# Optimization experiments

Measured on AMD Instinct MI355X. Metric: run time of the kernel, lower is better.

## Reference

```python
import jax, jax.numpy as jnp
import numpy as np

B, S, D, H, L, V = 4, 512, 1024, 16, 4, 32000
DH = D // H
LATENT_START, N_LATENT, LATENT_ID = 64, 6, 5


def _ln(x, g, b):
    m = x.mean(-1, keepdims=True)
    v = ((x - m) ** 2).mean(-1, keepdims=True)
    return (x - m) * jax.lax.rsqrt(v + 1e-5) * g + b


def _model(x_emb, pos_ids, pos_emb, Wqkv, Wo, W1, W2, ln1_g, ln1_b, ln2_g, ln2_b, lnf_g, lnf_b, lm_head):
    # x_emb: [B,T,D]; returns (last_hidden [B,T,D] after final LN, logits [B,T,V])
    b, T, _ = x_emb.shape
    x = x_emb + pos_emb[pos_ids]
    causal = jnp.tril(jnp.ones((T, T), bool))
    for l in range(L):
        h = _ln(x, ln1_g[l], ln1_b[l])
        q, k, v = jnp.split(h @ Wqkv[l], 3, axis=-1)
        q = q.reshape(b, T, H, DH).transpose(0, 2, 1, 3)
        k = k.reshape(b, T, H, DH).transpose(0, 2, 1, 3)
        v = v.reshape(b, T, H, DH).transpose(0, 2, 1, 3)
        scores = jnp.einsum('bhqd,bhkd->bhqk', q, k) / np.float32(np.sqrt(DH))
        scores = jnp.where(causal, scores, jnp.float32(-1e9))
        attn = jax.nn.softmax(scores, axis=-1)
        o = jnp.einsum('bhqk,bhkd->bhqd', attn, v).transpose(0, 2, 1, 3).reshape(b, T, D)
        x = x + o @ Wo[l]
        h2 = _ln(x, ln2_g[l], ln2_b[l])
        x = x + jax.nn.gelu(h2 @ W1[l]) @ W2[l]
    hid = _ln(x, lnf_g, lnf_b)  # GPT2 hidden_states[-1] is post ln_f
    return hid, hid @ lm_head


def setup_inputs() -> dict:
    key = jax.random.key(0)
    ks = jax.random.split(key, 10)
    input_ids = jax.random.randint(ks[0], (B, S), 0, V, dtype=jnp.int32)
    input_ids = input_ids.at[:, LATENT_START:LATENT_START + N_LATENT].set(LATENT_ID)
    attention_mask = jnp.ones((B, S), jnp.int32)
    labels = jax.random.randint(ks[1], (B, S), 0, V, dtype=jnp.int32)
    position_ids = jnp.broadcast_to(jnp.arange(S, dtype=jnp.int32), (B, S))
    s = 0.02
    return {
        'input_ids': input_ids, 'attention_mask': attention_mask,
        'labels': labels, 'position_ids': position_ids,
        'emb': jax.random.normal(ks[2], (V, D), jnp.float32) * s,
        'pos_emb': jax.random.normal(ks[3], (S, D), jnp.float32) * s,
        'Wqkv': jax.random.normal(ks[4], (L, D, 3 * D), jnp.float32) * s,
        'Wo': jax.random.normal(ks[5], (L, D, D), jnp.float32) * s,
        'W1': jax.random.normal(ks[6], (L, D, 4 * D), jnp.float32) * s,
        'W2': jax.random.normal(ks[7], (L, 4 * D, D), jnp.float32) * s,
        'ln1_g': jnp.ones((L, D), jnp.float32), 'ln1_b': jnp.zeros((L, D), jnp.float32),
        'ln2_g': jnp.ones((L, D), jnp.float32), 'ln2_b': jnp.zeros((L, D), jnp.float32),
        'lnf_g': jnp.ones((D,), jnp.float32), 'lnf_b': jnp.zeros((D,), jnp.float32),
        'lm_head': jax.random.normal(ks[8], (D, V), jnp.float32) * s,
    }


def reference(input_ids, attention_mask, labels, position_ids, emb, pos_emb, Wqkv, Wo, W1, W2, ln1_g, ln1_b, ln2_g, ln2_b, lnf_g, lnf_b, lm_head):
    params = (pos_emb, Wqkv, Wo, W1, W2, ln1_g, ln1_b, ln2_g, ln2_b, lnf_g, lnf_b, lm_head)
    inputs_embeds = emb[input_ids]  # [B,S,D]
    start, end = 0, LATENT_START
    logits_list = []
    for p in range(N_LATENT):  # iterative latent passes
        hid, lg = _model(inputs_embeds[:, :end], position_ids[:, :end], *params)
        logits_list.append(lg[:, start:end])
        pos = LATENT_START + p
        # vectorized scatter: splice previous-position hidden state into latent slot
        inputs_embeds = inputs_embeds.at[:, pos, :].set(hid[:, pos - 1, :])
        start, end = end, (S if p + 1 >= N_LATENT else end + 1)
    hid, lg = _model(inputs_embeds[:, :end], position_ids[:, :end], *params)
    logits_list.append(lg[:, start:end])
    logits = jnp.concatenate(logits_list, axis=1)  # [B,S,V]
    shift_logits = logits[:, :-1]
    shift_labels = labels[:, 1:]
    logp = jax.nn.log_softmax(shift_logits, axis=-1)
    loss = -jnp.take_along_axis(logp, shift_labels[..., None], axis=-1).mean()
    return loss, inputs_embeds, logits
```

## Files before the change

### kernel.cpp

```cpp
#include <hip/hip_runtime.h>

static constexpr int BB  = 4;
static constexpr int SS  = 512;
static constexpr int DD  = 1024;
static constexpr int HH  = 16;
static constexpr int LL  = 4;
static constexpr int VV  = 32000;
static constexpr int DHH = 64;
static constexpr int FFF = 4096;

typedef short bf16x8  __attribute__((ext_vector_type(8)));
typedef short bf16x4v __attribute__((ext_vector_type(4)));
typedef float f32x4   __attribute__((ext_vector_type(4)));

__device__ __forceinline__ float b2f(ushort u){
  union { float f; unsigned int u32; } x; x.u32 = ((unsigned int)u) << 16; return x.f;
}
__device__ __forceinline__ ushort f2b(float f){
  union { float f; unsigned int u32; } x; x.f = f;
  unsigned int u = x.u32;
  return (ushort)((u + 0x7FFFu + ((u >> 16) & 1u)) >> 16);
}

__device__ __forceinline__ void gl_lds16(const void* gp, void* lp){
  __builtin_amdgcn_global_load_lds((const __attribute__((address_space(1))) unsigned int*)gp,
                                   (__attribute__((address_space(3))) unsigned int*)lp, 16, 0, 0);
}

__device__ __forceinline__ bf16x4v lds_read4(const void* buf, int row, int col){
  int byte = row * 128 + (((((col >> 3) ^ (row & 7)) << 4) | ((col & 7) << 1)));
  return *(const bf16x4v*)((const char*)buf + byte);
}

__global__ __launch_bounds__(256) void convT_k(const float* __restrict__ in, ushort* __restrict__ out,
                                               int K, int N, long inStride, long outStride)
{
  in  += (long)blockIdx.z * inStride;
  out += (long)blockIdx.z * outStride;
  __shared__ float tile[64][65];
  int n0 = blockIdx.x * 64, k0 = blockIdx.y * 64;
  int tid = threadIdx.x;
  int cc = tid & 63, rr = tid >> 6;
#pragma unroll
  for (int i = 0; i < 16; i++){
    int r = rr + i * 4;
    tile[r][cc] = in[(long)(k0 + r) * N + n0 + cc];
  }
  __syncthreads();
#pragma unroll
  for (int i = 0; i < 16; i++){
    int r = rr + i * 4;
    out[(long)(n0 + r) * K + k0 + cc] = f2b(tile[cc][r]);
  }
}

__global__ __launch_bounds__(256) void embed_k(const int* __restrict__ ids, const float* __restrict__ emb,
                                               const float* __restrict__ pe, float* __restrict__ x,
                                               float* __restrict__ oemb)
{
  int t = blockIdx.x, b = blockIdx.y, tid = threadIdx.x;
  int id = ids[b * SS + t];
  float4 ev = *((const float4*)(emb + (long)id * DD) + tid);
  float4 pv = *((const float4*)(pe  + (long)t  * DD) + tid);
  *((float4*)(x + (long)(t * BB + b) * DD) + tid) =
      make_float4(ev.x + pv.x, ev.y + pv.y, ev.z + pv.z, ev.w + pv.w);
  float* op = oemb + ((long)b * SS + t) * DD + tid * 4;
  op[0] = ev.x; op[1] = ev.y; op[2] = ev.z; op[3] = ev.w;
}

__global__ __launch_bounds__(256) void ln_k(const float* __restrict__ xin, const float* __restrict__ g,
                                            const float* __restrict__ bt, ushort* __restrict__ out, long row0)
{
  long row = row0 + blockIdx.x;
  int tid = threadIdx.x;
  const float* rp = xin + row * DD;
  float4 v = *(const float4*)(rp + tid * 4);
  float s1 = v.x + v.y + v.z + v.w;
  float s2 = v.x * v.x + v.y * v.y + v.z * v.z + v.w * v.w;
#pragma unroll
  for (int o = 32; o; o >>= 1){ s1 += __shfl_down(s1, o); s2 += __shfl_down(s2, o); }
  __shared__ float red[2][4];
  int wv = tid >> 6, lane = tid & 63;
  if (lane == 0){ red[0][wv] = s1; red[1][wv] = s2; }
  __syncthreads();
  s1 = red[0][0] + red[0][1] + red[0][2] + red[0][3];
  s2 = red[1][0] + red[1][1] + red[1][2] + red[1][3];
  float mean = s1 * (1.0f / DD);
  float var  = s2 * (1.0f / DD) - mean * mean;
  float rstd = rsqrtf(var + 1e-5f);
  float4 gv = *(const float4*)(g + tid * 4);
  float4 bv = *(const float4*)(bt + tid * 4);
  ushort4 o4;
  o4.x = f2b((v.x - mean) * rstd * gv.x + bv.x);
  o4.y = f2b((v.y - mean) * rstd * gv.y + bv.y);
  o4.z = f2b((v.z - mean) * rstd * gv.z + bv.z);
  o4.w = f2b((v.w - mean) * rstd * gv.w + bv.w);
  *(ushort4*)(out + row * DD + tid * 4) = o4;
}

template<int EPI>
__device__ __forceinline__ void epi_store(float v, int grow, int ocol, void* Cv, int ldc,
                                          const float* Add, int t0, int l,
                                          ushort* kc, ushort* vc, ushort* qb)
{
  if constexpr (EPI == 1){
    float* Cf = (float*)Cv; long idx = (long)grow * ldc + ocol;
    Cf[idx] = v + Add[idx];
  } else if constexpr (EPI == 2){
    ushort* Cb = (ushort*)Cv; long idx = (long)grow * ldc + ocol;
    float tt = 0.7978845608028654f * (v + 0.044715f * v * v * v);
    Cb[idx] = f2b(0.5f * v * (1.0f + tanhf(tt)));
  } else if constexpr (EPI == 3){
    int t = t0 + (grow >> 2), b = grow & 3;
    ((float*)Cv)[((long)b * SS + t) * VV + ocol] = v;
  } else if constexpr (EPI == 4){
    if (ocol < DD){
      qb[((long)(t0 * BB + grow)) * DD + ocol] = f2b(v);
    } else {
      int t = t0 + (grow >> 2), b = grow & 3;
      int h = (ocol >> 6) & 15, d = ocol & 63;
      long dst = (((long)l * BB + b) * HH + h) * ((long)SS * DHH) + (long)t * DHH + d;
      if (ocol >= 2 * DD) vc[dst] = f2b(v); else kc[dst] = f2b(v);
    }
  }
}

template<int EPI>
__global__ __launch_bounds__(256) void gemm_k(const ushort* __restrict__ A, int lda,
                                              const ushort* __restrict__ BT,
                                              void* Cv, int ldc,
                                              const float* Add,
                                              int M, int N, int K, int gx,
                                              int l, int t0,
                                              ushort* kc, ushort* vc, ushort* qb,
                                              float* part, int KS)
{
  constexpr int BM  = 128;
  constexpr int MFR = 4;
  constexpr int NFR = 4;
  __shared__ ushort As[BM][64];
  __shared__ ushort Bs[128][64];
  int tid = threadIdx.x;
  int wv = tid >> 6, lane = tid & 63;
  int wm = wv >> 1, wn = wv & 1;

  int nwg = gridDim.x, orig = blockIdx.x;
  int qq = nwg >> 3, rr8 = nwg & 7, xcd = orig & 7;
  int wgid = ((xcd < rr8) ? xcd * (qq + 1) : rr8 * (qq + 1) + (xcd - rr8) * qq) + (orig >> 3);

  int gxy = gx * (N >> 7);
  int ksId = wgid / gxy;
  int rem  = wgid - ksId * gxy;
  int bx = rem % gx, by = rem / gx;
  int m0 = bx * BM, n0 = by * 128;
  int Kc = K / KS;
  int k_beg = ksId * Kc, k_end = k_beg + Kc;

  f32x4 acc[MFR][NFR];
  f32x4 zz = {0.f, 0.f, 0.f, 0.f};
#pragma unroll
  for (int m = 0; m < MFR; m++)
#pragma unroll
    for (int n = 0; n < NFR; n++) acc[m][n] = zz;

  int g4 = (lane >> 4) * 4;
  int rA = lane & 15;
  char* AsB = (char*)&As[0][0];
  char* BsB = (char*)&Bs[0][0];
  int arow = tid >> 3;
  int acol = (((tid & 7) ^ (arow & 7)) * 8);

  for (int k0 = k_beg; k0 < k_end; k0 += 64){
#pragma unroll
    for (int p = 0; p < 4; p++){
      int r = p * 32 + arow;
      gl_lds16(BT + (long)(n0 + r) * K + k0 + acol, BsB + p * 4096 + tid * 16);
    }
#pragma unroll
    for (int p = 0; p < 4; p++){
      int gr = m0 + p * 32 + arow;
      if (gr > M - 1) gr = M - 1;
      gl_lds16(A + (long)gr * lda + k0 + acol, AsB + p * 4096 + tid * 16);
    }
    __syncthreads();
#pragma unroll
    for (int kk = 0; kk < 64; kk += 32){
      bf16x8 af[MFR], bfr[NFR];
#pragma unroll
      for (int m = 0; m < MFR; m++){
        int row = wm * 64 + m * 16 + rA;
        bf16x4v lo = lds_read4(AsB, row, kk + g4);
        bf16x4v hi = lds_read4(AsB, row, kk + 16 + g4);
        af[m] = __builtin_shufflevector(lo, hi, 0, 1, 2, 3, 4, 5, 6, 7);
      }
#pragma unroll
      for (int n = 0; n < NFR; n++){
        int row = wn * 64 + n * 16 + rA;
        bf16x4v lo = lds_read4(BsB, row, kk + g4);
        bf16x4v hi = lds_read4(BsB, row, kk + 16 + g4);
        bfr[n] = __builtin_shufflevector(lo, hi, 0, 1, 2, 3, 4, 5, 6, 7);
      }
#pragma unroll
      for (int m = 0; m < MFR; m++)
#pragma unroll
        for (int n = 0; n < NFR; n++)
          acc[m][n] = __builtin_amdgcn_mfma_f32_16x16x32_bf16(af[m], bfr[n], acc[m][n], 0, 0, 0);
    }
    __syncthreads();
  }

  int r4 = (lane >> 4) * 4;
#pragma unroll
  for (int m = 0; m < MFR; m++){
#pragma unroll
    for (int n = 0; n < NFR; n++){
      int orow = wm * 64 + m * 16 + r4;
      int ocol = n0 + wn * 64 + n * 16 + rA;
#pragma unroll
      for (int r = 0; r < 4; r++){
        int grow = m0 + orow + r;
        if (grow < M){
          if (KS > 1)
            part[(long)ksId * M * N + (long)grow * N + ocol] = acc[m][n][r];
          else
            epi_store<EPI>(acc[m][n][r], grow, ocol, Cv, ldc, Add, t0, l, kc, vc, qb);
        }
      }
    }
  }
}

template<int EPI>
__global__ __launch_bounds__(256) void sred_k(const float* __restrict__ part, int KS, int M, int N,
                                              void* Cv, int ldc, const float* Add,
                                              int l, int t0, ushort* kc, ushort* vc, ushort* qb)
{
  long i = (long)blockIdx.x * 256 + threadIdx.x;
  long MN = (long)M * N;
  if (i >= MN) return;
  float v = 0.f;
  for (int s = 0; s < KS; s++) v += part[s * MN + i];
  int m = (int)(i / N), n = (int)(i - (long)m * N);
  epi_store<EPI>(v, m, n, Cv, ldc, Add, t0, l, kc, vc, qb);
}

template<int TYPE>
__global__ __launch_bounds__(256) void dec_gemv_k(const float* xf, const ushort* ab,
                                                  const float* g, const float* bt,
                                                  const ushort* WT, float* x,
                                                  ushort* qb, ushort* kc, ushort* vc, ushort* gb,
                                                  int l, int pos)
{
  constexpr int K   = (TYPE == 3) ? FFF : DD;
  constexpr int NCH = K / 1024;
  int tid = threadIdx.x, wid = tid >> 6, lane = tid & 63;
  int n = blockIdx.x * 4 + wid;

  float acc[4] = {0.f, 0.f, 0.f, 0.f};

#pragma unroll
  for (int ch = 0; ch < NCH; ch++){
    int ks = ch * 1024 + lane * 16;
    float a[4][16];
    if constexpr (TYPE == 0 || TYPE == 2){
#pragma unroll
      for (int r = 0; r < 4; r++){
        const float* rp = xf + (long)(pos * BB + r) * DD + ks;
#pragma unroll
        for (int q = 0; q < 4; q++){
          float4 v = *(const float4*)(rp + q * 4);
          a[r][q*4+0] = v.x; a[r][q*4+1] = v.y; a[r][q*4+2] = v.z; a[r][q*4+3] = v.w;
        }
      }
      float gj[16], bj[16];
#pragma unroll
      for (int q = 0; q < 4; q++){
        float4 gv = *(const float4*)(g  + ks + q * 4);
        float4 bv = *(const float4*)(bt + ks + q * 4);
        gj[q*4+0]=gv.x; gj[q*4+1]=gv.y; gj[q*4+2]=gv.z; gj[q*4+3]=gv.w;
        bj[q*4+0]=bv.x; bj[q*4+1]=bv.y; bj[q*4+2]=bv.z; bj[q*4+3]=bv.w;
      }
#pragma unroll
      for (int r = 0; r < 4; r++){
        float s1 = 0.f, s2 = 0.f;
#pragma unroll
        for (int j = 0; j < 16; j++){ s1 += a[r][j]; s2 += a[r][j] * a[r][j]; }
#pragma unroll
        for (int o = 32; o; o >>= 1){ s1 += __shfl_xor(s1, o); s2 += __shfl_xor(s2, o); }
        float mean = s1 * (1.0f / DD);
        float var  = s2 * (1.0f / DD) - mean * mean;
        float rstd = rsqrtf(var + 1e-5f);
#pragma unroll
        for (int j = 0; j < 16; j++)
          a[r][j] = b2f(f2b((a[r][j] - mean) * rstd * gj[j] + bj[j]));
      }
    } else {
      constexpr int AD = (TYPE == 3) ? FFF : DD;
#pragma unroll
      for (int r = 0; r < 4; r++){
        const ushort* rp = ab + (long)(pos * BB + r) * AD + ks;
        uint4 pa = *(const uint4*)rp;
        uint4 pb = *(const uint4*)(rp + 8);
        const unsigned int w[8] = {pa.x, pa.y, pa.z, pa.w, pb.x, pb.y, pb.z, pb.w};
#pragma unroll
        for (int q = 0; q < 8; q++){
          a[r][q*2]   = b2f((ushort)(w[q] & 0xffff));
          a[r][q*2+1] = b2f((ushort)(w[q] >> 16));
        }
      }
    }
    {
      const ushort* wp = WT + (long)n * K + ks;
      uint4 pa = *(const uint4*)wp;
      uint4 pb = *(const uint4*)(wp + 8);
      const unsigned int w[8] = {pa.x, pa.y, pa.z, pa.w, pb.x, pb.y, pb.z, pb.w};
      float wf[16];
#pragma unroll
      for (int q = 0; q < 8; q++){
        wf[q*2]   = b2f((ushort)(w[q] & 0xffff));
        wf[q*2+1] = b2f((ushort)(w[q] >> 16));
      }
#pragma unroll
      for (int r = 0; r < 4; r++){
        float s = 0.f;
#pragma unroll
        for (int j = 0; j < 16; j++) s += a[r][j] * wf[j];
        acc[r] += s;
      }
    }
  }

#pragma unroll
  for (int r = 0; r < 4; r++)
#pragma unroll
    for (int o = 32; o; o >>= 1) acc[r] += __shfl_xor(acc[r], o);

  if (lane < 4){
    int r = lane;
    long Rrow = (long)(pos * BB + r);
    float v = acc[r];
    if constexpr (TYPE == 0){
      if (n < DD){
        qb[Rrow * DD + n] = f2b(v);
      } else if (n < 2 * DD){
        int h = (n - DD) >> 6, d = n & 63;
        kc[(((long)l * BB + r) * HH + h) * ((long)SS * DHH) + (long)pos * DHH + d] = f2b(v);
      } else {
        int h = (n - 2 * DD) >> 6, d = n & 63;
        vc[(((long)l * BB + r) * HH + h) * ((long)SS * DHH) + (long)pos * DHH + d] = f2b(v);
      }
    } else if constexpr (TYPE == 2){
      float tt = 0.7978845608028654f * (v + 0.044715f * v * v * v);
      gb[Rrow * FFF + n] = f2b(0.5f * v * (1.0f + tanhf(tt)));
    } else {
      long idx = Rrow * DD + n;
      x[idx] = x[idx] + v;
    }
  }
}

__global__ __launch_bounds__(256) void dec_final_k(const float* xf, const float* g, const float* bt,
                                                   const float* pe, ushort* hid, float* x,
                                                   float* oemb, int pos)
{
  int wid = threadIdx.x >> 6, lane = threadIdx.x & 63;
  long R = (long)(pos * BB + wid);
  const float* rp = xf + R * DD + lane * 16;
  float a[16];
#pragma unroll
  for (int q = 0; q < 4; q++){
    float4 v = *(const float4*)(rp + q * 4);
    a[q*4+0] = v.x; a[q*4+1] = v.y; a[q*4+2] = v.z; a[q*4+3] = v.w;
  }
  float s1 = 0.f, s2 = 0.f;
#pragma unroll
  for (int j = 0; j < 16; j++){ s1 += a[j]; s2 += a[j] * a[j]; }
#pragma unroll
  for (int o = 32; o; o >>= 1){ s1 += __shfl_xor(s1, o); s2 += __shfl_xor(s2, o); }
  float mean = s1 * (1.0f / DD);
  float var  = s2 * (1.0f / DD) - mean * mean;
  float rstd = rsqrtf(var + 1e-5f);
  int pn = pos + 1;
#pragma unroll
  for (int j = 0; j < 16; j++){
    int d = lane * 16 + j;
    ushort hb = f2b((a[j] - mean) * rstd * g[d] + bt[d]);
    hid[R * DD + d] = hb;
    float hv = b2f(hb);
    oemb[((long)wid * SS + pn) * DD + d] = hv;
    x[((long)(pn * BB + wid)) * DD + d] = hv + pe[(long)pn * DD + d];
  }
}

__global__ __launch_bounds__(256) void attn_k(const ushort* __restrict__ qb, const ushort* __restrict__ kc,
                                              const ushort* __restrict__ vc, ushort* __restrict__ o,
                                              int l, int t0, int Tc)
{
  __shared__ float sc[4][512];
  __shared__ float qs[4][64];
  int tid = threadIdx.x, wv = tid >> 6, lane = tid & 63;
  int b = blockIdx.z, h = blockIdx.y;
  int qrow = blockIdx.x * 4 + wv;
  bool act = qrow < Tc;
  int tq = t0 + qrow;
  long kvoff = (((long)l * BB + b) * HH + h) * ((long)SS * DHH);
  const ushort* kb = kc + kvoff;
  const ushort* vb = vc + kvoff;
  if (act) qs[wv][lane] = b2f(qb[((long)(tq * BB + b)) * DD + h * DHH + lane]);
  __syncthreads();
  int nk = act ? (tq + 1) : 0;
  float m = -3.0e38f;
  for (int key = lane; key < nk; key += 64){
    const ushort* kp = kb + (long)key * DHH;
    float s = 0.f;
#pragma unroll
    for (int j = 0; j < 8; j++){
      uint4 kvv = *(const uint4*)(kp + j * 8);
      s += qs[wv][j*8+0] * b2f((ushort)(kvv.x & 0xffff));
      s += qs[wv][j*8+1] * b2f((ushort)(kvv.x >> 16));
      s += qs[wv][j*8+2] * b2f((ushort)(kvv.y & 0xffff));
      s += qs[wv][j*8+3] * b2f((ushort)(kvv.y >> 16));
      s += qs[wv][j*8+4] * b2f((ushort)(kvv.z & 0xffff));
      s += qs[wv][j*8+5] * b2f((ushort)(kvv.z >> 16));
      s += qs[wv][j*8+6] * b2f((ushort)(kvv.w & 0xffff));
      s += qs[wv][j*8+7] * b2f((ushort)(kvv.w >> 16));
    }
    s *= 0.125f;
    sc[wv][key] = s;
    m = fmaxf(m, s);
  }
#pragma unroll
  for (int off = 32; off; off >>= 1) m = fmaxf(m, __shfl_xor(m, off));
  float ssum = 0.f;
  for (int key = lane; key < nk; key += 64){
    float p = expf(sc[wv][key] - m);
    sc[wv][key] = p;
    ssum += p;
  }
#pragma unroll
  for (int off = 32; off; off >>= 1) ssum += __shfl_xor(ssum, off);
  __syncthreads();
  float accv = 0.f;
  int key = 0;
  for (; key + 3 < nk; key += 4){
    float p0 = sc[wv][key],     p1 = sc[wv][key + 1];
    float p2 = sc[wv][key + 2], p3 = sc[wv][key + 3];
    float v0 = b2f(vb[(long)key * DHH + lane]);
    float v1 = b2f(vb[(long)(key + 1) * DHH + lane]);
    float v2 = b2f(vb[(long)(key + 2) * DHH + lane]);
    float v3 = b2f(vb[(long)(key + 3) * DHH + lane]);
    accv += p0 * v0 + p1 * v1 + p2 * v2 + p3 * v3;
  }
  for (; key < nk; key++)
    accv += sc[wv][key] * b2f(vb[(long)key * DHH + lane]);
  if (act) o[((long)(tq * BB + b)) * DD + h * DHH + lane] = f2b(accv / ssum);
}

__global__ __launch_bounds__(256) void advance_k(const ushort* __restrict__ hid, const float* __restrict__ pe,
                                                 float* __restrict__ x, float* __restrict__ oemb, int pos)
{
  int d = blockIdx.x * 256 + threadIdx.x;
  int b = blockIdx.y;
  float hv = b2f(hid[((long)((pos - 1) * BB + b)) * DD + d]);
  oemb[((long)b * SS + pos) * DD + d] = hv;
  x[((long)(pos * BB + b)) * DD + d] = hv + pe[(long)pos * DD + d];
}

__global__ __launch_bounds__(256) void loss_rows_k(const float* __restrict__ logits, const int* __restrict__ labels,
                                                   float* __restrict__ rowloss)
{
  int t = blockIdx.x, b = blockIdx.y, tid = threadIdx.x;
  const float* row = logits + ((long)b * SS + t) * VV;
  float m = -3.0e38f, s = 0.f;
  for (int i = tid; i < VV; i += 256){
    float v = row[i];
    if (v > m){ s = s * expf(m - v) + 1.f; m = v; }
    else s += expf(v - m);
  }
#pragma unroll
  for (int off = 32; off; off >>= 1){
    float om = __shfl_xor(m, off), os = __shfl_xor(s, off);
    float nm = fmaxf(m, om);
    s = s * expf(m - nm) + os * expf(om - nm);
    m = nm;
  }
  __shared__ float sm[4], ssb[4];
  if ((tid & 63) == 0){ sm[tid >> 6] = m; ssb[tid >> 6] = s; }
  __syncthreads();
  if (tid == 0){
    float M = fmaxf(fmaxf(sm[0], sm[1]), fmaxf(sm[2], sm[3]));
    float S = ssb[0] * expf(sm[0] - M) + ssb[1] * expf(sm[1] - M)
            + ssb[2] * expf(sm[2] - M) + ssb[3] * expf(sm[3] - M);
    int lab = labels[b * SS + t + 1];
    rowloss[b * (SS - 1) + t] = (M + logf(S)) - row[lab];
  }
}

__global__ __launch_bounds__(256) void loss_final_k(const float* __restrict__ rowloss, float* __restrict__ out)
{
  int tid = threadIdx.x;
  float s = 0.f;
  for (int i = tid; i < BB * (SS - 1); i += 256) s += rowloss[i];
#pragma unroll
  for (int o = 32; o; o >>= 1) s += __shfl_down(s, o);
  __shared__ float red[4];
  if ((tid & 63) == 0) red[tid >> 6] = s;
  __syncthreads();
  if (tid == 0) out[0] = (red[0] + red[1] + red[2] + red[3]) / (float)(BB * (SS - 1));
}

static inline int cdiv_i(int a, int b){ return (a + b - 1) / b; }

extern "C" void kernel_launch(void* const* d_in, const int* in_sizes, int n_in,
                              void* d_out, int out_size, void* d_ws, size_t ws_size,
                              hipStream_t stream)
{
  (void)in_sizes; (void)n_in; (void)out_size; (void)ws_size;
  const int*   ids    = (const int*)d_in[0];
  const int*   labels = (const int*)d_in[2];
  const float* emb    = (const float*)d_in[4];
  const float* pe     = (const float*)d_in[5];
  const float* Wqkv   = (const float*)d_in[6];
  const float* Wo     = (const float*)d_in[7];
  const float* W1     = (const float*)d_in[8];
  const float* W2     = (const float*)d_in[9];
  const float* ln1g   = (const float*)d_in[10];
  const float* ln1b   = (const float*)d_in[11];
  const float* ln2g   = (const float*)d_in[12];
  const float* ln2b   = (const float*)d_in[13];
  const float* lnfg   = (const float*)d_in[14];
  const float* lnfb   = (const float*)d_in[15];
  const float* lm     = (const float*)d_in[16];

  float* out_loss   = (float*)d_out;
  float* out_emb    = out_loss + 1;
  float* out_logits = out_emb + (size_t)BB * SS * DD;

  char* wsp = (char*)d_ws;
  size_t off = 0;
  auto alloc = [&](size_t bytes) -> void* {
    void* p = wsp + off; off += (bytes + 255) & ~(size_t)255; return p;
  };
  ushort* wqkvT = (ushort*)alloc((size_t)LL * 3 * DD * DD * 2);
  ushort* woT   = (ushort*)alloc((size_t)LL * DD * DD * 2);
  ushort* w1T   = (ushort*)alloc((size_t)LL * FFF * DD * 2);
  ushort* w2T   = (ushort*)alloc((size_t)LL * DD * FFF * 2);
  ushort* lmT   = (ushort*)alloc((size_t)VV * DD * 2);
  float*  x     = (float*)alloc((size_t)BB * SS * DD * 4);
  ushort* hbuf  = (ushort*)alloc((size_t)BB * SS * DD * 2);
  ushort* qbuf  = (ushort*)alloc((size_t)BB * SS * DD * 2);
  ushort* obuf  = (ushort*)alloc((size_t)BB * SS * DD * 2);
  ushort* gbuf  = (ushort*)alloc((size_t)BB * SS * FFF * 2);
  ushort* hid   = (ushort*)alloc((size_t)BB * SS * DD * 2);
  ushort* kcache= (ushort*)alloc((size_t)LL * BB * SS * DD * 2);
  ushort* vcache= (ushort*)alloc((size_t)LL * BB * SS * DD * 2);
  float*  part  = (float*)alloc((size_t)17 * 1024 * 1024);
  float*  rowls = (float*)alloc((size_t)BB * (SS - 1) * 4);

  convT_k<<<dim3(3 * DD / 64, DD / 64, LL), dim3(256), 0, stream>>>(Wqkv, wqkvT, DD, 3 * DD, (long)DD * 3 * DD, (long)3 * DD * DD);
  convT_k<<<dim3(DD / 64, DD / 64, LL),     dim3(256), 0, stream>>>(Wo,   woT,  DD, DD,     (long)DD * DD,     (long)DD * DD);
  convT_k<<<dim3(FFF / 64, DD / 64, LL),    dim3(256), 0, stream>>>(W1,   w1T,  DD, FFF,    (long)DD * FFF,    (long)FFF * DD);
  convT_k<<<dim3(DD / 64, FFF / 64, LL),    dim3(256), 0, stream>>>(W2,   w2T,  FFF, DD,    (long)FFF * DD,    (long)DD * FFF);
  convT_k<<<dim3(VV / 64, DD / 64, 1),      dim3(256), 0, stream>>>(lm,   lmT,  DD, VV,     0, 0);

  embed_k<<<dim3(SS, BB), dim3(256), 0, stream>>>(ids, emb, pe, x, out_emb);

  const int ct0[7] = {0, 64, 65, 66, 67, 68, 69};
  const int ct1[7] = {64, 65, 66, 67, 68, 69, 512};

  auto g128 = [&](int epi, const ushort* A, int lda, const ushort* BT, void* C, int ldc,
                  const float* Add, int M, int N, int K, int l, int t0, int KS){
    int gx = cdiv_i(M, 128);
    int nwg = gx * (N >> 7) * KS;
    if (epi == 1) gemm_k<1><<<nwg, 256, 0, stream>>>(A, lda, BT, C, ldc, Add, M, N, K, gx, l, t0, kcache, vcache, qbuf, part, KS);
    if (epi == 2) gemm_k<2><<<nwg, 256, 0, stream>>>(A, lda, BT, C, ldc, Add, M, N, K, gx, l, t0, kcache, vcache, qbuf, part, KS);
    if (epi == 3) gemm_k<3><<<nwg, 256, 0, stream>>>(A, lda, BT, C, ldc, Add, M, N, K, gx, l, t0, kcache, vcache, qbuf, part, KS);
    if (epi == 4) gemm_k<4><<<nwg, 256, 0, stream>>>(A, lda, BT, C, ldc, Add, M, N, K, gx, l, t0, kcache, vcache, qbuf, part, KS);
    if (KS > 1){
      int nred = cdiv_i(M * N, 256);
      if (epi == 1) sred_k<1><<<nred, 256, 0, stream>>>(part, KS, M, N, C, ldc, Add, l, t0, kcache, vcache, qbuf);
      if (epi == 2) sred_k<2><<<nred, 256, 0, stream>>>(part, KS, M, N, C, ldc, Add, l, t0, kcache, vcache, qbuf);
      if (epi == 4) sred_k<4><<<nred, 256, 0, stream>>>(part, KS, M, N, C, ldc, Add, l, t0, kcache, vcache, qbuf);
    }
  };

  for (int c = 0; c < 7; c++){
    int t0 = ct0[c];
    int Tc = ct1[c] - t0;
    int M  = Tc * BB;
    long roff = (long)t0 * BB;

    if (Tc == 1){
      int pos = t0;
      for (int l = 0; l < LL; l++){
        dec_gemv_k<0><<<dim3(3 * DD / 4), dim3(256), 0, stream>>>(x, nullptr, ln1g + l * DD, ln1b + l * DD,
            wqkvT + (long)l * 3 * DD * DD, nullptr, qbuf, kcache, vcache, nullptr, l, pos);
        attn_k<<<dim3(1, HH, BB), dim3(64), 0, stream>>>(qbuf, kcache, vcache, obuf, l, t0, Tc);
        dec_gemv_k<1><<<dim3(DD / 4), dim3(256), 0, stream>>>(nullptr, obuf, nullptr, nullptr,
            woT + (long)l * DD * DD, x, nullptr, nullptr, nullptr, nullptr, l, pos);
        dec_gemv_k<2><<<dim3(FFF / 4), dim3(256), 0, stream>>>(x, nullptr, ln2g + l * DD, ln2b + l * DD,
            w1T + (long)l * FFF * DD, nullptr, nullptr, nullptr, nullptr, gbuf, l, pos);
        dec_gemv_k<3><<<dim3(DD / 4), dim3(256), 0, stream>>>(nullptr, gbuf, nullptr, nullptr,
            w2T + (long)l * DD * FFF, x, nullptr, nullptr, nullptr, nullptr, l, pos);
      }
      dec_final_k<<<dim3(1), dim3(256), 0, stream>>>(x, lnfg, lnfb, pe, hid, x, out_emb, pos);
    } else {
      bool small = (M <= 256);
      int ksQKV = small ? 4 : 1;
      int ksWO  = small ? 8 : 2;
      int ksW1  = small ? 4 : 1;
      int ksW2  = small ? 8 : 2;
      for (int l = 0; l < LL; l++){
        ln_k<<<dim3(M), dim3(256), 0, stream>>>(x, ln1g + l * DD, ln1b + l * DD, hbuf, roff);
        g128(4, hbuf + roff * DD, DD, wqkvT + (long)l * 3 * DD * DD, nullptr, 0, nullptr, M, 3 * DD, DD, l, t0, ksQKV);
        attn_k<<<dim3(cdiv_i(Tc, 4), HH, BB), dim3(256), 0, stream>>>(qbuf, kcache, vcache, obuf, l, t0, Tc);
        g128(1, obuf + roff * DD, DD, woT + (long)l * DD * DD, x + roff * DD, DD, x + roff * DD, M, DD, DD, l, t0, ksWO);
        ln_k<<<dim3(M), dim3(256), 0, stream>>>(x, ln2g + l * DD, ln2b + l * DD, hbuf, roff);
        g128(2, hbuf + roff * DD, DD, w1T + (long)l * FFF * DD, gbuf + roff * FFF, FFF, nullptr, M, FFF, DD, l, t0, ksW1);
        g128(1, gbuf + roff * FFF, FFF, w2T + (long)l * DD * FFF, x + roff * DD, DD, x + roff * DD, M, DD, FFF, l, t0, ksW2);
      }
      ln_k<<<dim3(M), dim3(256), 0, stream>>>(x, lnfg, lnfb, hid, roff);
      if (c == 0)
        advance_k<<<dim3(DD / 256, BB), dim3(256), 0, stream>>>(hid, pe, x, out_emb, 64);
    }
  }

  g128(3, hid, DD, lmT, out_logits, 0, nullptr, BB * SS, VV, DD, 0, 0, 1);

  loss_rows_k<<<dim3(SS - 1, BB), dim3(256), 0, stream>>>(out_logits, labels, rowls);
  loss_final_k<<<dim3(1), dim3(256), 0, stream>>>(rowls, out_loss);
}
```

Measured before the change: 2.956 ms.

## Prefetch GEMM tiles into registers and use padded LDS instead of direct global-to-LDS loads

```diff
diff --git a/kernel.cpp b/kernel.cpp
--- a/kernel.cpp
+++ b/kernel.cpp
@@ -20,16 +20,6 @@
   union { float f; unsigned int u32; } x; x.f = f;
   unsigned int u = x.u32;
   return (ushort)((u + 0x7FFFu + ((u >> 16) & 1u)) >> 16);
-}
-
-__device__ __forceinline__ void gl_lds16(const void* gp, void* lp){
-  __builtin_amdgcn_global_load_lds((const __attribute__((address_space(1))) unsigned int*)gp,
-                                   (__attribute__((address_space(3))) unsigned int*)lp, 16, 0, 0);
-}
-
-__device__ __forceinline__ bf16x4v lds_read4(const void* buf, int row, int col){
-  int byte = row * 128 + (((((col >> 3) ^ (row & 7)) << 4) | ((col & 7) << 1)));
-  return *(const bf16x4v*)((const char*)buf + byte);
 }
 
 __global__ __launch_bounds__(256) void convT_k(const float* __restrict__ in, ushort* __restrict__ out,
@@ -138,8 +128,8 @@
   constexpr int BM  = 128;
   constexpr int MFR = 4;
   constexpr int NFR = 4;
-  __shared__ ushort As[BM][64];
-  __shared__ ushort Bs[128][64];
+  __shared__ ushort As[BM][72];
+  __shared__ ushort Bs[128][72];
   int tid = threadIdx.x;
   int wv = tid >> 6, lane = tid & 63;
   int wm = wv >> 1, wn = wv & 1;
@@ -165,39 +155,48 @@
 
   int g4 = (lane >> 4) * 4;
   int rA = lane & 15;
-  char* AsB = (char*)&As[0][0];
-  char* BsB = (char*)&Bs[0][0];
   int arow = tid >> 3;
-  int acol = (((tid & 7) ^ (arow & 7)) * 8);
-
-  for (int k0 = k_beg; k0 < k_end; k0 += 64){
+  int acol = (tid & 7) * 8;
+
+  uint4 bufA[4], bufB[4];
+  auto load_tiles = [&](int k0){
 #pragma unroll
     for (int p = 0; p < 4; p++){
       int r = p * 32 + arow;
-      gl_lds16(BT + (long)(n0 + r) * K + k0 + acol, BsB + p * 4096 + tid * 16);
-    }
+      bufB[p] = *(const uint4*)(BT + (long)(n0 + r) * K + k0 + acol);
+      int gr = m0 + r;
+      uint4 av = make_uint4(0u, 0u, 0u, 0u);
+      if (gr < M) av = *(const uint4*)(A + (long)gr * lda + k0 + acol);
+      bufA[p] = av;
+    }
+  };
+
+  load_tiles(k_beg);
+
+  for (int k0 = k_beg; k0 < k_end; k0 += 64){
 #pragma unroll
     for (int p = 0; p < 4; p++){
-      int gr = m0 + p * 32 + arow;
-      if (gr > M - 1) gr = M - 1;
-      gl_lds16(A + (long)gr * lda + k0 + acol, AsB + p * 4096 + tid * 16);
+      int r = p * 32 + arow;
+      *(uint4*)&Bs[r][acol] = bufB[p];
+      *(uint4*)&As[r][acol] = bufA[p];
     }
     __syncthreads();
+    if (k0 + 64 < k_end) load_tiles(k0 + 64);
 #pragma unroll
     for (int kk = 0; kk < 64; kk += 32){
       bf16x8 af[MFR], bfr[NFR];
 #pragma unroll
       for (int m = 0; m < MFR; m++){
         int row = wm * 64 + m * 16 + rA;
-        bf16x4v lo = lds_read4(AsB, row, kk + g4);
-        bf16x4v hi = lds_read4(AsB, row, kk + 16 + g4);
+        bf16x4v lo = *(const bf16x4v*)&As[row][kk + g4];
+        bf16x4v hi = *(const bf16x4v*)&As[row][kk + 16 + g4];
         af[m] = __builtin_shufflevector(lo, hi, 0, 1, 2, 3, 4, 5, 6, 7);
       }
 #pragma unroll
       for (int n = 0; n < NFR; n++){
         int row = wn * 64 + n * 16 + rA;
-        bf16x4v lo = lds_read4(BsB, row, kk + g4);
-        bf16x4v hi = lds_read4(BsB, row, kk + 16 + g4);
+        bf16x4v lo = *(const bf16x4v*)&Bs[row][kk + g4];
+        bf16x4v hi = *(const bf16x4v*)&Bs[row][kk + 16 + g4];
         bfr[n] = __builtin_shufflevector(lo, hi, 0, 1, 2, 3, 4, 5, 6, 7);
       }
 #pragma unroll
```

Measured after the change: 3.776 ms. 1.28x slower.
